# Kernel tuning notes

Hardware: AMD Instinct MI355X
Metric: run time of the kernel (lower is better)

## Reference

```python
import jax, jax.numpy as jnp
import numpy as np

N_HEAD = 4
HIDDEN = 1024
D_HEAD = HIDDEN // N_HEAD  # 256
SEQ = 1024
BATCH = 16
NEG_INF = -1e9


def setup_inputs() -> dict:
    key = jax.random.key(0)
    k1, k2, k3 = jax.random.split(key, 3)
    x = jax.random.normal(k1, (BATCH, SEQ, HIDDEN), dtype=jnp.float32)
    # torch Linear(hidden, (2n+1)*d_head, bias=False); stored here as [in, out]
    w_qkv = jax.random.normal(k2, (HIDDEN, (2 * N_HEAD + 1) * D_HEAD), dtype=jnp.float32) * (HIDDEN ** -0.5)
    # out_proj: Linear(d_head, hidden, bias=False), stored as [d_head, hidden]
    w_out = jax.random.normal(k3, (D_HEAD, HIDDEN), dtype=jnp.float32) * (D_HEAD ** -0.5)
    return {"x": x, "w_qkv": w_qkv, "w_out": w_out}


def reference(x, w_qkv, w_out):
    bs, t, h = x.shape
    n_head, d_head = N_HEAD, D_HEAD
    scale = d_head ** -0.5
    qkv = x @ w_qkv  # [bs, t, (2n+1)*d]
    q = qkv[..., : n_head * d_head].reshape(bs, t, n_head, d_head)
    k = qkv[..., n_head * d_head : 2 * n_head * d_head].reshape(bs, t, n_head, d_head)
    v = qkv[..., 2 * n_head * d_head :]  # [bs, t, d] -- single shared V
    # scores [bs, n_head, t, s]
    scores = jnp.einsum("btnd,bsnd->bnts", q, k) * scale
    causal = jnp.triu(jnp.ones((t, t), dtype=bool), 1)  # True above diag
    scores = jnp.where(causal, NEG_INF, scores)
    attn_prob = jax.nn.softmax(scores, axis=-1)  # [bs, n_head, t, s]
    attn_vec = jnp.einsum("bnts,bsd->bntd", attn_prob, v)
    m_attn_vec = jnp.mean(attn_vec, axis=1)  # mean over heads -> [bs, t, d]
    out = m_attn_vec @ w_out  # [bs, t, hidden]
    return out, attn_prob
```

## Files before the change

kernel.cpp:

```cpp
#include <hip/hip_runtime.h>
#include <hip/hip_bf16.h>
#include <type_traits>

#define BATCH  16
#define SEQ    1024
#define HIDDEN 1024
#define NHEAD  4
#define DHEAD  256
#define QKVN   2304

typedef _Float16 f16x8 __attribute__((ext_vector_type(8)));
typedef float    f32x4 __attribute__((ext_vector_type(4)));

__device__ __forceinline__ void gll16(const void* g, void* l) {
  __builtin_amdgcn_global_load_lds(
      (const __attribute__((address_space(1))) unsigned int*)g,
      (__attribute__((address_space(3))) unsigned int*)l, 16, 0, 0);
}

__global__ __launch_bounds__(256) void f32_to_f16(
    const float* __restrict__ in, _Float16* __restrict__ out) {
  int i4 = blockIdx.x * 256 + threadIdx.x;
  float4 v = ((const float4*)in)[i4];
  _Float16 h4[4] = {(_Float16)v.x, (_Float16)v.y, (_Float16)v.z, (_Float16)v.w};
  *(uint2*)&out[(size_t)i4 * 4] = *(uint2*)h4;
}

__global__ __launch_bounds__(256) void transpose_to_f16(
    const float* __restrict__ in, _Float16* __restrict__ out, int R, int C) {
  __shared__ float tile[64][65];
  int bc = blockIdx.x * 64, br = blockIdx.y * 64;
  int t = threadIdx.x;
  int tr = t >> 6, tc = t & 63;
  for (int i = 0; i < 64; i += 4)
    tile[tr + i][tc] = in[(size_t)(br + tr + i) * C + bc + tc];
  __syncthreads();
  for (int i = 0; i < 64; i += 4)
    out[(size_t)(bc + tr + i) * R + br + tc] = (_Float16)tile[tc][tr + i];
}

__global__ __launch_bounds__(256) void transpose_v(
    const _Float16* __restrict__ qkv, _Float16* __restrict__ vT) {
  __shared__ _Float16 tile[64][65];
  int b = blockIdx.z;
  int s0 = blockIdx.x * 64, d0 = blockIdx.y * 64;
  int t = threadIdx.x;
  int tr = t >> 6, tc = t & 63;
  for (int i = 0; i < 64; i += 4)
    tile[tr + i][tc] = qkv[((size_t)(b * SEQ + s0 + tr + i)) * QKVN + 2 * NHEAD * DHEAD + d0 + tc];
  __syncthreads();
  for (int i = 0; i < 64; i += 4)
    vT[((size_t)(b * DHEAD + d0 + tr + i)) * SEQ + s0 + tc] = tile[tc][tr + i];
}

template <typename OT>
__global__ __launch_bounds__(256) void gemm_bt(
    const _Float16* __restrict__ A, const _Float16* __restrict__ B,
    OT* __restrict__ C, int M, int N, int K) {
  __shared__ __align__(16) _Float16 As[128][32];
  __shared__ __align__(16) _Float16 Bs[128][32];
  int bm = blockIdx.x * 128, bn = blockIdx.y * 128;
  int t = threadIdx.x;
  int w = t >> 6, L = t & 63, lane15 = L & 15, quad = L >> 4;
  int wr = (w >> 1) * 64, wc = (w & 1) * 64;
  f32x4 acc[4][4] = {};
  for (int k0 = 0; k0 < K; k0 += 32) {
    __syncthreads();
    for (int r = 0; r < 2; r++) {
      int u = t + r * 256;
      int row = u >> 2, c8 = u & 3;
      gll16(&A[(size_t)(bm + row) * K + k0 + c8 * 8], &As[row][c8 * 8]);
      gll16(&B[(size_t)(bn + row) * K + k0 + c8 * 8], &Bs[row][c8 * 8]);
    }
    __syncthreads();
    f16x8 af[4], bf[4];
    for (int i = 0; i < 4; i++) af[i] = *(f16x8*)&As[wr + i * 16 + lane15][quad * 8];
    for (int j = 0; j < 4; j++) bf[j] = *(f16x8*)&Bs[wc + j * 16 + lane15][quad * 8];
    for (int i = 0; i < 4; i++)
      for (int j = 0; j < 4; j++)
        acc[i][j] = __builtin_amdgcn_mfma_f32_16x16x32_f16(af[i], bf[j], acc[i][j], 0, 0, 0);
  }
  for (int i = 0; i < 4; i++)
    for (int j = 0; j < 4; j++) {
      int gr = bm + wr + i * 16 + quad * 4;
      int gc = bn + wc + j * 16 + lane15;
      for (int r = 0; r < 4; r++) {
        float v = acc[i][j][r];
        if constexpr (std::is_same_v<OT, float>)
          C[(size_t)(gr + r) * N + gc] = v;
        else
          C[(size_t)(gr + r) * N + gc] = (_Float16)v;
      }
    }
}

__global__ __launch_bounds__(512) void scores_kernel(
    const _Float16* __restrict__ qkv, float* __restrict__ P,
    float* __restrict__ m_g, float* __restrict__ rl_g) {
  int ti = blockIdx.x, n = blockIdx.y, b = blockIdx.z;
  __shared__ __align__(16) _Float16 Qs[8][64][32];
  __shared__ __align__(16) _Float16 Ks[8][64][32];
  int t = threadIdx.x;
  int w = t >> 6, L = t & 63, lane15 = L & 15, quad = L >> 4;
  int r16 = (w & 3) * 16;
  int ch  = (w >> 2) * 32;
  for (int r = 0; r < 4; r++) {
    int u = t + r * 512;
    int kc = u >> 8, row = (u & 255) >> 2, c8 = u & 3;
    gll16(&qkv[((size_t)(b * SEQ + ti * 64 + row)) * QKVN + n * DHEAD + kc * 32 + c8 * 8],
          &Qs[kc][row][c8 * 8]);
  }
  float m[4], l[4];
  for (int r = 0; r < 4; r++) { m[r] = -INFINITY; l[r] = 0.f; }
  size_t Pbase = ((size_t)(b * NHEAD + n)) * SEQ * SEQ;
  int trow = ti * 64 + r16 + quad * 4;
  const float scale = 0.0625f;
  for (int si = 0; si <= ti; si++) {
    __syncthreads();
    for (int r = 0; r < 4; r++) {
      int u = t + r * 512;
      int kc = u >> 8, row = (u & 255) >> 2, c8 = u & 3;
      gll16(&qkv[((size_t)(b * SEQ + si * 64 + row)) * QKVN + NHEAD * DHEAD + n * DHEAD + kc * 32 + c8 * 8],
            &Ks[kc][row][c8 * 8]);
    }
    __syncthreads();
    f32x4 s[2] = {};
    for (int kc = 0; kc < 8; kc++) {
      f16x8 aq = *(f16x8*)&Qs[kc][r16 + lane15][quad * 8];
      for (int j = 0; j < 2; j++) {
        f16x8 bk = *(f16x8*)&Ks[kc][ch + j * 16 + lane15][quad * 8];
        s[j] = __builtin_amdgcn_mfma_f32_16x16x32_f16(aq, bk, s[j], 0, 0, 0);
      }
    }
    for (int j = 0; j < 2; j++) {
      int col = si * 64 + ch + j * 16 + lane15;
      for (int r = 0; r < 4; r++) {
        float v = s[j][r] * scale;
        if (col > trow + r) v = -1e9f;
        s[j][r] = v;
        P[Pbase + (size_t)(trow + r) * SEQ + col] = v;
      }
    }
    for (int r = 0; r < 4; r++) {
      float mt = fmaxf(s[0][r], s[1][r]);
      for (int off = 1; off < 16; off <<= 1) mt = fmaxf(mt, __shfl_xor(mt, off, 64));
      float mn = fmaxf(m[r], mt);
      float sum = __expf(s[0][r] - mn) + __expf(s[1][r] - mn);
      for (int off = 1; off < 16; off <<= 1) sum += __shfl_xor(sum, off, 64);
      l[r] = l[r] * __expf(m[r] - mn) + sum;
      m[r] = mn;
    }
  }
  __syncthreads();
  float* sM = (float*)&Qs[0][0][0];
  float* sL = sM + 128;
  if (lane15 == 0) {
    for (int r = 0; r < 4; r++) {
      sM[(w >> 2) * 64 + r16 + quad * 4 + r] = m[r];
      sL[(w >> 2) * 64 + r16 + quad * 4 + r] = l[r];
    }
  }
  __syncthreads();
  if (t < 64) {
    float m0 = sM[t], m1 = sM[64 + t], l0 = sL[t], l1 = sL[64 + t];
    float mc = fmaxf(m0, m1);
    float lc = l0 * __expf(m0 - mc) + l1 * __expf(m1 - mc);
    size_t idx = ((size_t)(b * NHEAD + n)) * SEQ + ti * 64 + t;
    m_g[idx] = mc;
    rl_g[idx] = 1.0f / lc;
  }
}

__global__ __launch_bounds__(256) void norm_mean_kernel(
    float* __restrict__ P, const float* __restrict__ m_g,
    const float* __restrict__ rl_g, _Float16* __restrict__ Pmean) {
  int si = blockIdx.x, ti = blockIdx.y, b = blockIdx.z;
  int t = threadIdx.x;
  int row = t >> 2, c16 = (t & 3) * 16;
  size_t tile_off = (size_t)(ti * 64 + row) * SEQ + si * 64 + c16;
  if (si > ti) {
    float4 z = make_float4(0.f, 0.f, 0.f, 0.f);
    for (int n = 0; n < 4; n++) {
      float* p = &P[((size_t)(b * NHEAD + n)) * SEQ * SEQ + tile_off];
      for (int q = 0; q < 4; q++) *(float4*)(p + q * 4) = z;
    }
    return;
  }
  float acc[16];
  for (int i = 0; i < 16; i++) acc[i] = 0.f;
  for (int n = 0; n < 4; n++) {
    size_t sidx = ((size_t)(b * NHEAD + n)) * SEQ + ti * 64 + row;
    float mm = m_g[sidx], rr = rl_g[sidx];
    float* p = &P[((size_t)(b * NHEAD + n)) * SEQ * SEQ + tile_off];
    for (int q = 0; q < 4; q++) {
      float4 v = *(float4*)(p + q * 4);
      float4 e;
      e.x = __expf(v.x - mm) * rr;
      e.y = __expf(v.y - mm) * rr;
      e.z = __expf(v.z - mm) * rr;
      e.w = __expf(v.w - mm) * rr;
      *(float4*)(p + q * 4) = e;
      acc[q * 4 + 0] += e.x; acc[q * 4 + 1] += e.y;
      acc[q * 4 + 2] += e.z; acc[q * 4 + 3] += e.w;
    }
  }
  _Float16 h[16];
  for (int i = 0; i < 16; i++) h[i] = (_Float16)(acc[i] * 0.25f);
  _Float16* pm = &Pmean[((size_t)(b * SEQ + ti * 64 + row)) * SEQ + si * 64 + c16];
  *(uint4*)pm = *(uint4*)h;
  *(uint4*)(pm + 8) = *(uint4*)(h + 8);
}

__global__ __launch_bounds__(256) void pv_kernel(
    const _Float16* __restrict__ Pmean, const _Float16* __restrict__ vT,
    _Float16* __restrict__ mattn) {
  int ti = blockIdx.x, b = blockIdx.y;
  __shared__ __align__(16) _Float16 Pm[2][64][32];
  __shared__ __align__(16) _Float16 Vs[2][256][32];
  int t = threadIdx.x;
  int w = t >> 6, L = t & 63, lane15 = L & 15, quad = L >> 4;
  f32x4 acc[16] = {};
  for (int si = 0; si <= ti; si++) {
    __syncthreads();
    for (int r = 0; r < 2; r++) {
      int u = t + r * 256;
      int kc = u >> 8, row = (u & 255) >> 2, c8 = u & 3;
      gll16(&Pmean[((size_t)(b * SEQ + ti * 64 + row)) * SEQ + si * 64 + kc * 32 + c8 * 8],
            &Pm[kc][row][c8 * 8]);
    }
    for (int r = 0; r < 8; r++) {
      int u = t + r * 256;
      int kc = u >> 10, d = (u & 1023) >> 2, c8 = u & 3;
      gll16(&vT[((size_t)(b * DHEAD + d)) * SEQ + si * 64 + kc * 32 + c8 * 8],
            &Vs[kc][d][c8 * 8]);
    }
    __syncthreads();
    for (int kc = 0; kc < 2; kc++) {
      f16x8 ap = *(f16x8*)&Pm[kc][w * 16 + lane15][quad * 8];
      for (int j = 0; j < 16; j++) {
        f16x8 bv = *(f16x8*)&Vs[kc][j * 16 + lane15][quad * 8];
        acc[j] = __builtin_amdgcn_mfma_f32_16x16x32_f16(ap, bv, acc[j], 0, 0, 0);
      }
    }
  }
  for (int j = 0; j < 16; j++) {
    int row = b * SEQ + ti * 64 + w * 16 + quad * 4;
    int col = j * 16 + lane15;
    for (int r = 0; r < 4; r++)
      mattn[(size_t)(row + r) * DHEAD + col] = (_Float16)acc[j][r];
  }
}

extern "C" void kernel_launch(void* const* d_in, const int* in_sizes, int n_in,
                              void* d_out, int out_size, void* d_ws, size_t ws_size,
                              hipStream_t stream) {
  const float* x     = (const float*)d_in[0];
  const float* w_qkv = (const float*)d_in[1];
  const float* w_out = (const float*)d_in[2];
  float* out = (float*)d_out;
  float* P   = out + (size_t)BATCH * SEQ * HIDDEN;

  _Float16* wqkvT = (_Float16*)d_ws;
  _Float16* woutT = wqkvT + (size_t)QKVN * HIDDEN;
  _Float16* qkvb  = woutT + (size_t)HIDDEN * DHEAD;
  _Float16* vT    = qkvb + (size_t)BATCH * SEQ * QKVN;
  float*    m_g   = (float*)(vT + (size_t)BATCH * DHEAD * SEQ);
  float*    rl_g  = m_g + (size_t)BATCH * NHEAD * SEQ;
  _Float16* mattn = qkvb;
  _Float16* Pmean = qkvb + (size_t)BATCH * SEQ * DHEAD;
  _Float16* xh    = (_Float16*)P;

  f32_to_f16<<<BATCH * SEQ * HIDDEN / 1024, 256, 0, stream>>>(x, xh);
  transpose_to_f16<<<dim3(QKVN / 64, HIDDEN / 64), 256, 0, stream>>>(w_qkv, wqkvT, HIDDEN, QKVN);
  transpose_to_f16<<<dim3(HIDDEN / 64, DHEAD / 64), 256, 0, stream>>>(w_out, woutT, DHEAD, HIDDEN);
  gemm_bt<_Float16><<<dim3(BATCH * SEQ / 128, QKVN / 128), 256, 0, stream>>>(
      xh, wqkvT, qkvb, BATCH * SEQ, QKVN, HIDDEN);
  transpose_v<<<dim3(SEQ / 64, DHEAD / 64, BATCH), 256, 0, stream>>>(qkvb, vT);
  scores_kernel<<<dim3(SEQ / 64, NHEAD, BATCH), 512, 0, stream>>>(qkvb, P, m_g, rl_g);
  norm_mean_kernel<<<dim3(SEQ / 64, SEQ / 64, BATCH), 256, 0, stream>>>(P, m_g, rl_g, Pmean);
  pv_kernel<<<dim3(SEQ / 64, BATCH), 256, 0, stream>>>(Pmean, vT, mattn);
  gemm_bt<float><<<dim3(BATCH * SEQ / 128, HIDDEN / 128), 256, 0, stream>>>(
      mattn, woutT, out, BATCH * SEQ, HIDDEN, DHEAD);
}
```

Baseline: 763.5 us.

## Keep raw scores in registers and write normalized probabilities directly from scores kernel

The scores kernel now holds all 16 score tiles per row block in registers. After computing the row max and sum, it applies the exp-normalization and writes final probabilities to P once, also zeroing the upper-triangular region itself. This removes the write of raw scores followed by a read-modify-write pass over P in the separate normalization kernel. The mean kernel now only reads P to build Pmean. The cost is heavy register pressure (128 floats of scores per thread, unrolled), which can spill and lower occupancy.

```diff
diff --git a/kernel.cpp b/kernel.cpp
--- a/kernel.cpp
+++ b/kernel.cpp
@@ -94,9 +94,8 @@
     }
 }
 
-__global__ __launch_bounds__(512) void scores_kernel(
-    const _Float16* __restrict__ qkv, float* __restrict__ P,
-    float* __restrict__ m_g, float* __restrict__ rl_g) {
+__global__ __launch_bounds__(512, 2) void scores_norm_kernel(
+    const _Float16* __restrict__ qkv, float* __restrict__ P) {
   int ti = blockIdx.x, n = blockIdx.y, b = blockIdx.z;
   __shared__ __align__(16) _Float16 Qs[8][64][32];
   __shared__ __align__(16) _Float16 Ks[8][64][32];
@@ -112,48 +111,53 @@
   }
   float m[4], l[4];
   for (int r = 0; r < 4; r++) { m[r] = -INFINITY; l[r] = 0.f; }
-  size_t Pbase = ((size_t)(b * NHEAD + n)) * SEQ * SEQ;
+  f32x4 s[16][2];
   int trow = ti * 64 + r16 + quad * 4;
   const float scale = 0.0625f;
-  for (int si = 0; si <= ti; si++) {
-    __syncthreads();
-    for (int r = 0; r < 4; r++) {
-      int u = t + r * 512;
-      int kc = u >> 8, row = (u & 255) >> 2, c8 = u & 3;
-      gll16(&qkv[((size_t)(b * SEQ + si * 64 + row)) * QKVN + NHEAD * DHEAD + n * DHEAD + kc * 32 + c8 * 8],
-            &Ks[kc][row][c8 * 8]);
-    }
-    __syncthreads();
-    f32x4 s[2] = {};
-    for (int kc = 0; kc < 8; kc++) {
-      f16x8 aq = *(f16x8*)&Qs[kc][r16 + lane15][quad * 8];
+#pragma unroll
+  for (int si = 0; si < 16; si++) {
+    if (si <= ti) {
+      __syncthreads();
+      for (int r = 0; r < 4; r++) {
+        int u = t + r * 512;
+        int kc = u >> 8, row = (u & 255) >> 2, c8 = u & 3;
+        gll16(&qkv[((size_t)(b * SEQ + si * 64 + row)) * QKVN + NHEAD * DHEAD + n * DHEAD + kc * 32 + c8 * 8],
+              &Ks[kc][row][c8 * 8]);
+      }
+      __syncthreads();
+      s[si][0] = (f32x4){0.f, 0.f, 0.f, 0.f};
+      s[si][1] = (f32x4){0.f, 0.f, 0.f, 0.f};
+      for (int kc = 0; kc < 8; kc++) {
+        f16x8 aq = *(f16x8*)&Qs[kc][r16 + lane15][quad * 8];
+        for (int j = 0; j < 2; j++) {
+          f16x8 bk = *(f16x8*)&Ks[kc][ch + j * 16 + lane15][quad * 8];
+          s[si][j] = __builtin_amdgcn_mfma_f32_16x16x32_f16(aq, bk, s[si][j], 0, 0, 0);
+        }
+      }
       for (int j = 0; j < 2; j++) {
-        f16x8 bk = *(f16x8*)&Ks[kc][ch + j * 16 + lane15][quad * 8];
-        s[j] = __builtin_amdgcn_mfma_f32_16x16x32_f16(aq, bk, s[j], 0, 0, 0);
-      }
-    }
-    for (int j = 0; j < 2; j++) {
-      int col = si * 64 + ch + j * 16 + lane15;
+        int col = si * 64 + ch + j * 16 + lane15;
+        for (int r = 0; r < 4; r++) {
+          float v = s[si][j][r] * scale;
+          if (col > trow + r) v = -1e9f;
+          s[si][j][r] = v;
+        }
+      }
       for (int r = 0; r < 4; r++) {
-        float v = s[j][r] * scale;
-        if (col > trow + r) v = -1e9f;
-        s[j][r] = v;
-        P[Pbase + (size_t)(trow + r) * SEQ + col] = v;
-      }
-    }
-    for (int r = 0; r < 4; r++) {
-      float mt = fmaxf(s[0][r], s[1][r]);
-      for (int off = 1; off < 16; off <<= 1) mt = fmaxf(mt, __shfl_xor(mt, off, 64));
-      float mn = fmaxf(m[r], mt);
-      float sum = __expf(s[0][r] - mn) + __expf(s[1][r] - mn);
-      for (int off = 1; off < 16; off <<= 1) sum += __shfl_xor(sum, off, 64);
-      l[r] = l[r] * __expf(m[r] - mn) + sum;
-      m[r] = mn;
-    }
-  }
-  __syncthreads();
-  float* sM = (float*)&Qs[0][0][0];
-  float* sL = sM + 128;
+        float mt = fmaxf(s[si][0][r], s[si][1][r]);
+        for (int off = 1; off < 16; off <<= 1) mt = fmaxf(mt, __shfl_xor(mt, off, 64));
+        float mn = fmaxf(m[r], mt);
+        float sum = __expf(s[si][0][r] - mn) + __expf(s[si][1][r] - mn);
+        for (int off = 1; off < 16; off <<= 1) sum += __shfl_xor(sum, off, 64);
+        l[r] = l[r] * __expf(m[r] - mn) + sum;
+        m[r] = mn;
+      }
+    }
+  }
+  __syncthreads();
+  float* sM  = (float*)&Qs[0][0][0];
+  float* sL  = sM + 128;
+  float* sMc = sM + 256;
+  float* sRl = sM + 320;
   if (lane15 == 0) {
     for (int r = 0; r < 4; r++) {
       sM[(w >> 2) * 64 + r16 + quad * 4 + r] = m[r];
@@ -165,43 +169,54 @@
     float m0 = sM[t], m1 = sM[64 + t], l0 = sL[t], l1 = sL[64 + t];
     float mc = fmaxf(m0, m1);
     float lc = l0 * __expf(m0 - mc) + l1 * __expf(m1 - mc);
-    size_t idx = ((size_t)(b * NHEAD + n)) * SEQ + ti * 64 + t;
-    m_g[idx] = mc;
-    rl_g[idx] = 1.0f / lc;
-  }
-}
-
-__global__ __launch_bounds__(256) void norm_mean_kernel(
-    float* __restrict__ P, const float* __restrict__ m_g,
-    const float* __restrict__ rl_g, _Float16* __restrict__ Pmean) {
+    sMc[t] = mc;
+    sRl[t] = 1.0f / lc;
+  }
+  __syncthreads();
+  float mr[4], rl[4];
+  for (int r = 0; r < 4; r++) {
+    mr[r] = sMc[r16 + quad * 4 + r];
+    rl[r] = sRl[r16 + quad * 4 + r];
+  }
+  size_t Pbase = ((size_t)(b * NHEAD + n)) * SEQ * SEQ;
+#pragma unroll
+  for (int si = 0; si < 16; si++) {
+    if (si <= ti) {
+      for (int j = 0; j < 2; j++) {
+        int col = si * 64 + ch + j * 16 + lane15;
+        for (int r = 0; r < 4; r++) {
+          float p = (col > trow + r) ? 0.f : __expf(s[si][j][r] - mr[r]) * rl[r];
+          P[Pbase + (size_t)(trow + r) * SEQ + col] = p;
+        }
+      }
+    }
+  }
+  {
+    float4 z = make_float4(0.f, 0.f, 0.f, 0.f);
+    int c4min = (ti + 1) * 16;
+    for (int u = t; u < 16384; u += 512) {
+      int row = u >> 8, c4 = u & 255;
+      if (c4 >= c4min)
+        *(float4*)&P[Pbase + (size_t)(ti * 64 + row) * SEQ + c4 * 4] = z;
+    }
+  }
+}
+
+__global__ __launch_bounds__(256) void pmean_kernel(
+    const float* __restrict__ P, _Float16* __restrict__ Pmean) {
   int si = blockIdx.x, ti = blockIdx.y, b = blockIdx.z;
+  if (si > ti) return;
   int t = threadIdx.x;
   int row = t >> 2, c16 = (t & 3) * 16;
   size_t tile_off = (size_t)(ti * 64 + row) * SEQ + si * 64 + c16;
-  if (si > ti) {
-    float4 z = make_float4(0.f, 0.f, 0.f, 0.f);
-    for (int n = 0; n < 4; n++) {
-      float* p = &P[((size_t)(b * NHEAD + n)) * SEQ * SEQ + tile_off];
-      for (int q = 0; q < 4; q++) *(float4*)(p + q * 4) = z;
-    }
-    return;
-  }
   float acc[16];
   for (int i = 0; i < 16; i++) acc[i] = 0.f;
   for (int n = 0; n < 4; n++) {
-    size_t sidx = ((size_t)(b * NHEAD + n)) * SEQ + ti * 64 + row;
-    float mm = m_g[sidx], rr = rl_g[sidx];
-    float* p = &P[((size_t)(b * NHEAD + n)) * SEQ * SEQ + tile_off];
+    const float* p = &P[((size_t)(b * NHEAD + n)) * SEQ * SEQ + tile_off];
     for (int q = 0; q < 4; q++) {
-      float4 v = *(float4*)(p + q * 4);
-      float4 e;
-      e.x = __expf(v.x - mm) * rr;
-      e.y = __expf(v.y - mm) * rr;
-      e.z = __expf(v.z - mm) * rr;
-      e.w = __expf(v.w - mm) * rr;
-      *(float4*)(p + q * 4) = e;
-      acc[q * 4 + 0] += e.x; acc[q * 4 + 1] += e.y;
-      acc[q * 4 + 2] += e.z; acc[q * 4 + 3] += e.w;
+      float4 v = *(const float4*)(p + q * 4);
+      acc[q * 4 + 0] += v.x; acc[q * 4 + 1] += v.y;
+      acc[q * 4 + 2] += v.z; acc[q * 4 + 3] += v.w;
     }
   }
   _Float16 h[16];
@@ -264,8 +279,6 @@
   _Float16* woutT = wqkvT + (size_t)QKVN * HIDDEN;
   _Float16* qkvb  = woutT + (size_t)HIDDEN * DHEAD;
   _Float16* vT    = qkvb + (size_t)BATCH * SEQ * QKVN;
-  float*    m_g   = (float*)(vT + (size_t)BATCH * DHEAD * SEQ);
-  float*    rl_g  = m_g + (size_t)BATCH * NHEAD * SEQ;
   _Float16* mattn = qkvb;
   _Float16* Pmean = qkvb + (size_t)BATCH * SEQ * DHEAD;
   _Float16* xh    = (_Float16*)P;
@@ -276,8 +289,8 @@
   gemm_bt<_Float16><<<dim3(BATCH * SEQ / 128, QKVN / 128), 256, 0, stream>>>(
       xh, wqkvT, qkvb, BATCH * SEQ, QKVN, HIDDEN);
   transpose_v<<<dim3(SEQ / 64, DHEAD / 64, BATCH), 256, 0, stream>>>(qkvb, vT);
-  scores_kernel<<<dim3(SEQ / 64, NHEAD, BATCH), 512, 0, stream>>>(qkvb, P, m_g, rl_g);
-  norm_mean_kernel<<<dim3(SEQ / 64, SEQ / 64, BATCH), 256, 0, stream>>>(P, m_g, rl_g, Pmean);
+  scores_norm_kernel<<<dim3(SEQ / 64, NHEAD, BATCH), 512, 0, stream>>>(qkvb, P);
+  pmean_kernel<<<dim3(SEQ / 64, SEQ / 64, BATCH), 256, 0, stream>>>(P, Pmean);
   pv_kernel<<<dim3(SEQ / 64, BATCH), 256, 0, stream>>>(Pmean, vT, mattn);
   gemm_bt<float><<<dim3(BATCH * SEQ / 128, HIDDEN / 128), 256, 0, stream>>>(
       mattn, woutT, out, BATCH * SEQ, HIDDEN, DHEAD);
```

Measured after the change: 728.9 us. 4.5% less time.
